# Kernel optimization log

Measured on AMD Instinct MI355X. Metric: run time of the kernel, lower is better.

The kernel has to match this reference:

```python
import jax, jax.numpy as jnp
import numpy as np

N_NODES = 50000


def graph_conv(x, W, b, src, dst, n_nodes):
    # DGL GraphConv with norm='both': h = D_in^{-1/2} A D_out^{-1/2} x W + b
    ones = jnp.ones(src.shape[0], dtype=x.dtype)
    deg_out = jax.ops.segment_sum(ones, src, num_segments=n_nodes)
    deg_in = jax.ops.segment_sum(ones, dst, num_segments=n_nodes)
    norm_out = jnp.power(jnp.clip(deg_out, 1.0, None), -0.5)
    norm_in = jnp.power(jnp.clip(deg_in, 1.0, None), -0.5)
    x = x * norm_out[:, None]
    msgs = x[src]                                   # [E, d] gather
    agg = jax.ops.segment_sum(msgs, dst, num_segments=n_nodes)  # [N, d] scatter-add
    agg = agg * norm_in[:, None]
    return agg @ W + b


def setup_inputs() -> dict:
    key = jax.random.key(0)
    ks = jax.random.split(key, 16)
    d = 128
    h = 2 * d
    od = 64
    E = 800000
    T = 4096

    def lin(k, fan_in, fan_out):
        bound = 1.0 / np.sqrt(fan_in)
        k1, k2 = jax.random.split(k)
        W = jax.random.uniform(k1, (fan_in, fan_out), jnp.float32, -bound, bound)
        b = jax.random.uniform(k2, (fan_out,), jnp.float32, -bound, bound)
        return W, b

    features = jax.random.normal(ks[0], (N_NODES, d), jnp.float32)
    src = jax.random.randint(ks[1], (E,), 0, N_NODES)
    dst = jax.random.randint(ks[2], (E,), 0, N_NODES)
    trigger_nodes = jax.random.randint(ks[3], (T,), 0, N_NODES)

    W1, b1 = lin(ks[4], d, h)
    W2, b2 = lin(ks[5], h, d)
    Wf, bf = lin(ks[6], d, d)
    Wf1, bf1 = lin(ks[7], d, d)
    We, be = lin(ks[8], d, od)
    We1, be1 = lin(ks[9], od, od)

    return {
        "features": features, "src": src, "dst": dst,
        "trigger_nodes": trigger_nodes,
        "W1": W1, "b1": b1, "W2": W2, "b2": b2,
        "Wf": Wf, "bf": bf, "Wf1": Wf1, "bf1": bf1,
        "We": We, "be": be, "We1": We1, "be1": be1,
    }


def reference(features, src, dst, trigger_nodes,
              W1, b1, W2, b2, Wf, bf, Wf1, bf1, We, be, We1, be1):
    n = features.shape[0]
    h = jax.nn.relu(graph_conv(features, W1, b1, src, dst, n))   # [N, 2d]
    h = jax.nn.relu(graph_conv(h, W2, b2, src, dst, n))          # [N, d]
    ht = h[trigger_nodes]                                        # [T, d] gather
    feat = jax.nn.relu(ht @ Wf + bf) @ Wf1 + bf1                 # [T, d]
    edge_weight = jax.nn.relu(ht @ We + be) @ We1 + be1          # [T, od]
    return (feat, edge_weight)
```

## Files before the change

### kernel.cpp

```cpp
#include <hip/hip_runtime.h>
#include <hip/hip_bf16.h>


typedef __attribute__((ext_vector_type(8))) short short8;
typedef __attribute__((ext_vector_type(4))) float f32x4;

#define NQ_CAP 12544

union U16B { uint4 u; short8 s; };

__device__ __forceinline__ unsigned pack_hl(float v)
{
    unsigned u = __builtin_bit_cast(unsigned, v);
    unsigned rb = u + 0x7fffu + ((u >> 16) & 1u);
    float hf = __builtin_bit_cast(float, rb & 0xffff0000u);
    float r = v - hf;
    unsigned l = __builtin_bit_cast(unsigned, r) & 0xffff0000u;
    return (rb >> 16) | l;
}

__device__ __forceinline__ float decode_hl(unsigned u)
{
    float hf = __builtin_bit_cast(float, u << 16);
    float lf = __builtin_bit_cast(float, u & 0xffff0000u);
    return hf + lf;
}

__device__ __forceinline__ void unpack_hl(uint4 a, uint4 b, short8& h, short8& l)
{
    U16B H, L;
    H.u.x = (a.x & 0xffffu) | (a.y << 16);
    H.u.y = (a.z & 0xffffu) | (a.w << 16);
    H.u.z = (b.x & 0xffffu) | (b.y << 16);
    H.u.w = (b.z & 0xffffu) | (b.w << 16);
    L.u.x = (a.x >> 16) | (a.y & 0xffff0000u);
    L.u.y = (a.z >> 16) | (a.w & 0xffff0000u);
    L.u.z = (b.x >> 16) | (b.y & 0xffff0000u);
    L.u.w = (b.z >> 16) | (b.w & 0xffff0000u);
    h = H.s; l = L.s;
}

__global__ __launch_bounds__(256) void hist_kernel(
    const int* __restrict__ src, const int* __restrict__ dst,
    unsigned* __restrict__ part_in, unsigned* __restrict__ part_out,
    int E, int chunk, int nq)
{
    __shared__ unsigned c32[NQ_CAP];
    const int b = blockIdx.x;
    const int* __restrict__ idx = blockIdx.y ? src : dst;
    unsigned* __restrict__ part = blockIdx.y ? part_out : part_in;

    for (int i = threadIdx.x; i < nq; i += 256) c32[i] = 0u;
    __syncthreads();

    const int base = b * chunk;
    const int lim = min(base + chunk, E);
    for (int e = base + threadIdx.x; e < lim; e += 256) {
        int n = idx[e];
        atomicAdd(&c32[n >> 2], 1u << ((n & 3) * 8));
    }
    __syncthreads();

    unsigned* __restrict__ o = part + (long)b * nq;
    for (int i = threadIdx.x; i < nq; i += 256) o[i] = c32[i];
}

__global__ __launch_bounds__(256) void merge_kernel(
    unsigned* __restrict__ part_in, const unsigned* __restrict__ part_out,
    int* __restrict__ deg_in, float* __restrict__ norm_in,
    float* __restrict__ norm_out, int nq, int N)
{
    __shared__ unsigned gsum[4][64];
    const int il = threadIdx.x & 63;
    const int bg = threadIdx.x >> 6;
    const int i = blockIdx.x * 64 + il;
    const bool valid = (i < nq);

    unsigned p[32];
    unsigned run = 0u;
    if (valid) {
        #pragma unroll
        for (int j = 0; j < 32; ++j)
            p[j] = part_in[(long)(bg * 32 + j) * nq + i];
        #pragma unroll
        for (int j = 0; j < 32; ++j) run += p[j];
    }
    gsum[bg][il] = run;
    __syncthreads();

    unsigned base = 0u;
    #pragma unroll
    for (int g = 0; g < 4; ++g) {
        unsigned v = gsum[g][il];
        if (g < bg) base += v;
    }

    unsigned ro = 0u;
    if (valid) {
        #pragma unroll
        for (int j = 0; j < 32; ++j)
            ro += part_out[(long)(bg * 32 + j) * nq + i];
    }

    if (valid) {
        unsigned acc = base;
        #pragma unroll
        for (int j = 0; j < 32; ++j) {
            part_in[(long)(bg * 32 + j) * nq + i] = acc;
            acc += p[j];
        }
        if (bg == 3) {
            #pragma unroll
            for (int k = 0; k < 4; ++k) {
                int n = 4 * i + k;
                if (n < N) {
                    int dk = (int)((acc >> (8 * k)) & 0xffu);
                    deg_in[n] = dk;
                    norm_in[n] = rsqrtf(fmaxf((float)dk, 1.0f));
                }
            }
        }
    }

    __syncthreads();
    gsum[bg][il] = ro;
    __syncthreads();
    if (valid && bg == 0) {
        unsigned rt = gsum[0][il] + gsum[1][il] + gsum[2][il] + gsum[3][il];
        #pragma unroll
        for (int k = 0; k < 4; ++k) {
            int n = 4 * i + k;
            if (n < N)
                norm_out[n] = rsqrtf(fmaxf((float)((rt >> (8 * k)) & 0xffu), 1.0f));
        }
    }
}

__global__ __launch_bounds__(256) void scan1_kernel(
    const int* __restrict__ deg, int* __restrict__ rowptr,
    int* __restrict__ bsum, int N)
{
    __shared__ int s[256];
    int t = threadIdx.x;
    int i = blockIdx.x * 256 + t;
    s[t] = (i < N) ? deg[i] : 0;
    __syncthreads();
    #pragma unroll
    for (int off = 1; off < 256; off <<= 1) {
        int v = (t >= off) ? s[t - off] : 0;
        __syncthreads();
        s[t] += v;
        __syncthreads();
    }
    if (i < N) rowptr[i + 1] = s[t];
    if (t == 255) bsum[blockIdx.x] = s[255];
}

__global__ __launch_bounds__(256) void scan2_kernel(int* __restrict__ bsum, int nb)
{
    __shared__ int s[256];
    int t = threadIdx.x;
    s[t] = (t < nb) ? bsum[t] : 0;
    __syncthreads();
    #pragma unroll
    for (int off = 1; off < 256; off <<= 1) {
        int v = (t >= off) ? s[t - off] : 0;
        __syncthreads();
        s[t] += v;
        __syncthreads();
    }
    if (t < nb) bsum[t] = s[t];
}

__global__ __launch_bounds__(256) void scan3_kernel(
    int* __restrict__ rowptr, const int* __restrict__ bsum, int N)
{
    int b = blockIdx.x;
    int i = b * 256 + threadIdx.x;
    if (i < N) {
        int add = (b > 0) ? bsum[b - 1] : 0;
        rowptr[i + 1] += add;
    }
    if (i == 0) rowptr[0] = 0;
}

__global__ __launch_bounds__(256) void fill2_kernel(
    const int* __restrict__ src, const int* __restrict__ dst,
    const int* __restrict__ rowptr, const unsigned* __restrict__ part_in,
    int* __restrict__ ecol, int E, int chunk, int nq)
{
    __shared__ unsigned c32[NQ_CAP];
    const int b = blockIdx.x;
    const unsigned* __restrict__ pref = part_in + (long)b * nq;
    for (int i = threadIdx.x; i < nq; i += 256) c32[i] = pref[i];
    __syncthreads();

    const int base = b * chunk;
    const int lim = min(base + chunk, E);
    for (int e = base + threadIdx.x; e < lim; e += 256) {
        int r = dst[e];
        unsigned old = atomicAdd(&c32[r >> 2], 1u << ((r & 3) * 8));
        unsigned slot = (old >> ((r & 3) * 8)) & 0xffu;
        ecol[rowptr[r] + (int)slot] = src[e];
    }
}

struct WPrep {
    const float* w[6];
    unsigned* o[6];
    int K[6], N[6], dstK[6], base[7];
};

__global__ __launch_bounds__(256) void wprep_kernel(WPrep p)
{
    int t = blockIdx.x * 256 + threadIdx.x;
    if (t >= p.base[6]) return;
    int s = 0;
    while (t >= p.base[s + 1]) ++s;
    int loc = t - p.base[s];
    int K = p.K[s], N = p.N[s];
    int n = loc / K, k = loc - n * K;
    p.o[s][(long)n * p.dstK[s] + k] = pack_hl(p.w[s][(long)k * N + n]);
}

__global__ __launch_bounds__(256) void gather4_kernel(
    const float* __restrict__ x, const float* __restrict__ nsrc,
    const int* __restrict__ rowptr, const int* __restrict__ ecol,
    unsigned* __restrict__ out, int N)
{
    const int wave = threadIdx.x >> 6;
    const int lane = threadIdx.x & 63;
    const int r = blockIdx.x * 4 + wave;
    if (r >= N) return;
    const int q = lane & 31;
    const int h = lane >> 5;
    const int beg = rowptr[r], end = rowptr[r + 1];
    const float4* __restrict__ x4 = (const float4*)x;

    float4 acc = make_float4(0.f, 0.f, 0.f, 0.f);
    int k = beg + h;
    int sA = (k < end) ? ecol[k] : -1;
    int sB = (k + 2 < end) ? ecol[k + 2] : -1;
    float4 vA = make_float4(0.f, 0.f, 0.f, 0.f), vB = vA;
    float nA = 0.f, nB = 0.f;
    if (sA >= 0) { vA = x4[(long)sA * 32 + q]; nA = nsrc[sA]; }
    if (sB >= 0) { vB = x4[(long)sB * 32 + q]; nB = nsrc[sB]; }
    while (sA >= 0) {
        int sC = (k + 4 < end) ? ecol[k + 4] : -1;
        float4 vC = make_float4(0.f, 0.f, 0.f, 0.f);
        float nC = 0.f;
        if (sC >= 0) { vC = x4[(long)sC * 32 + q]; nC = nsrc[sC]; }
        acc.x = fmaf(vA.x, nA, acc.x);
        acc.y = fmaf(vA.y, nA, acc.y);
        acc.z = fmaf(vA.z, nA, acc.z);
        acc.w = fmaf(vA.w, nA, acc.w);
        sA = sB; vA = vB; nA = nB;
        sB = sC; vB = vC; nB = nC;
        k += 2;
    }
    acc.x += __shfl(acc.x, lane ^ 32);
    acc.y += __shfl(acc.y, lane ^ 32);
    acc.z += __shfl(acc.z, lane ^ 32);
    acc.w += __shfl(acc.w, lane ^ 32);
    if (h == 0) {
        uint4 o;
        o.x = pack_hl(acc.x); o.y = pack_hl(acc.y);
        o.z = pack_hl(acc.z); o.w = pack_hl(acc.w);
        *reinterpret_cast<uint4*>(&out[(long)r * 128 + q * 4]) = o;
    }
}

__global__ __launch_bounds__(256) void gather_trig256_kernel(
    const unsigned* __restrict__ h1s, const int* __restrict__ trig,
    const float* __restrict__ norm_in,
    const int* __restrict__ rowptr, const int* __restrict__ ecol,
    unsigned* __restrict__ agg2ts, int T)
{
    const int wave = threadIdx.x >> 6;
    const int lane = threadIdx.x & 63;
    const int b = blockIdx.x * 4 + wave;
    if (b >= T) return;
    const int r = trig[b];
    const int beg = rowptr[r], end = rowptr[r + 1];
    const uint4* __restrict__ h4 = (const uint4*)h1s;

    float4 acc = make_float4(0.f, 0.f, 0.f, 0.f);
    int k = beg;
    int sA = (k < end) ? ecol[k] : -1;
    int sB = (k + 1 < end) ? ecol[k + 1] : -1;
    uint4 vA = make_uint4(0u, 0u, 0u, 0u), vB = vA;
    if (sA >= 0) vA = h4[(long)sA * 64 + lane];
    if (sB >= 0) vB = h4[(long)sB * 64 + lane];
    while (sA >= 0) {
        int sC = (k + 2 < end) ? ecol[k + 2] : -1;
        uint4 vC = make_uint4(0u, 0u, 0u, 0u);
        if (sC >= 0) vC = h4[(long)sC * 64 + lane];
        acc.x += decode_hl(vA.x);
        acc.y += decode_hl(vA.y);
        acc.z += decode_hl(vA.z);
        acc.w += decode_hl(vA.w);
        sA = sB; vA = vB;
        sB = sC; vB = vC;
        ++k;
    }
    const float ni = norm_in[r];
    uint4 o;
    o.x = pack_hl(acc.x * ni); o.y = pack_hl(acc.y * ni);
    o.z = pack_hl(acc.z * ni); o.w = pack_hl(acc.w * ni);
    *reinterpret_cast<uint4*>(&agg2ts[(long)b * 256 + lane * 4]) = o;
}

__global__ __launch_bounds__(256) void mgemm256_kernel(
    const unsigned* __restrict__ A, const unsigned* __restrict__ Bp,
    const float* __restrict__ bias, const float* __restrict__ ni,
    const float* __restrict__ no, unsigned* __restrict__ Cp, int M)
{
    constexpr int K = 128;
    const int tid = threadIdx.x;
    const int lane = tid & 63, wave = tid >> 6;
    const int l15 = lane & 15, l4 = lane >> 4;
    const int row0 = blockIdx.x * 128;

    long aof[2];
    #pragma unroll
    for (int i = 0; i < 2; ++i) {
        int r = row0 + wave * 32 + i * 16 + l15;
        if (r > M - 1) r = M - 1;
        aof[i] = (long)r * K + l4 * 8;
    }
    const long bbase = (long)l15 * K + l4 * 8;

    uint4 abuf[2][2][2];
    #pragma unroll
    for (int i = 0; i < 2; ++i) {
        abuf[0][i][0] = *reinterpret_cast<const uint4*>(&A[aof[i] + 0]);
        abuf[0][i][1] = *reinterpret_cast<const uint4*>(&A[aof[i] + 4]);
        abuf[1][i][0] = *reinterpret_cast<const uint4*>(&A[aof[i] + 32]);
        abuf[1][i][1] = *reinterpret_cast<const uint4*>(&A[aof[i] + 36]);
    }

    f32x4 acc[2][16];
    #pragma unroll
    for (int i = 0; i < 2; ++i)
        #pragma unroll
        for (int j = 0; j < 16; ++j)
            acc[i][j] = (f32x4){0.f, 0.f, 0.f, 0.f};

    uint4 bq[4][2];
    #pragma unroll
    for (int t0 = 0; t0 < 4; ++t0) {
        const long na = bbase + (long)(t0 & 15) * 16 * K + (t0 >> 4) * 32;
        bq[t0][0] = *reinterpret_cast<const uint4*>(&Bp[na]);
        bq[t0][1] = *reinterpret_cast<const uint4*>(&Bp[na + 4]);
    }

    short8 ah[2], al[2];

    #pragma unroll
    for (int t = 0; t < 64; ++t) {
        const int c = t >> 4, j = t & 15;
        if (j == 0) {
            const int cp = c & 1;
            unpack_hl(abuf[cp][0][0], abuf[cp][0][1], ah[0], al[0]);
            unpack_hl(abuf[cp][1][0], abuf[cp][1][1], ah[1], al[1]);
            if (c + 2 < 4) {
                #pragma unroll
                for (int i = 0; i < 2; ++i) {
                    abuf[cp][i][0] = *reinterpret_cast<const uint4*>(&A[aof[i] + (c + 2) * 32]);
                    abuf[cp][i][1] = *reinterpret_cast<const uint4*>(&A[aof[i] + (c + 2) * 32 + 4]);
                }
            }
        }
        short8 bh, bl;
        unpack_hl(bq[t & 3][0], bq[t & 3][1], bh, bl);
        if (t + 4 < 64) {
            const int c1 = (t + 4) >> 4, j1 = (t + 4) & 15;
            const long na = bbase + (long)j1 * 16 * K + c1 * 32;
            bq[t & 3][0] = *reinterpret_cast<const uint4*>(&Bp[na]);
            bq[t & 3][1] = *reinterpret_cast<const uint4*>(&Bp[na + 4]);
        }
        #pragma unroll
        for (int i = 0; i < 2; ++i) {
            acc[i][j] = __builtin_amdgcn_mfma_f32_16x16x32_bf16(ah[i], bh, acc[i][j], 0, 0, 0);
            acc[i][j] = __builtin_amdgcn_mfma_f32_16x16x32_bf16(ah[i], bl, acc[i][j], 0, 0, 0);
            acc[i][j] = __builtin_amdgcn_mfma_f32_16x16x32_bf16(al[i], bh, acc[i][j], 0, 0, 0);
        }
    }

    #pragma unroll
    for (int i = 0; i < 2; ++i) {
        const int rbase = row0 + wave * 32 + i * 16 + l4 * 4;
        #pragma unroll
        for (int g = 0; g < 4; ++g) {
            const int row = rbase + g;
            if (row >= M) continue;
            const float niv = ni[row], nov = no[row];
            #pragma unroll
            for (int j = 0; j < 16; ++j) {
                const int col = j * 16 + l15;
                float v = fmaxf(fmaf(niv, acc[i][j][g], bias[col]), 0.f) * nov;
                Cp[(long)row * 256 + col] = pack_hl(v);
            }
        }
    }
}

template<int TN, bool RELU, bool PACK_OUT>
__global__ __launch_bounds__(256) void mgemm_kernel(
    const unsigned* __restrict__ A, const unsigned* __restrict__ Bp,
    const float* __restrict__ bias, const float* __restrict__ bias2,
    const float* __restrict__ rowscale, const float* __restrict__ outscale,
    float* __restrict__ C, unsigned* __restrict__ Cp, int M, int N, int K)
{
    constexpr int IM = 2, KC = 32, TM = 128;
    constexpr int JF = TN / 16;
    constexpr int BLD = (TN * KC) / (4 * 256);

    __shared__ unsigned sB[KC * TN];

    const int tid = threadIdx.x;
    const int lane = tid & 63;
    const int wave = tid >> 6;
    const int l15 = lane & 15, l4 = lane >> 4;
    const int row0 = blockIdx.y * TM;
    const int col0 = blockIdx.x * TN;

    int bro[BLD], bgr[BLD];
    long bof[BLD];
    #pragma unroll
    for (int l = 0; l < BLD; ++l) {
        int idx = tid + 256 * l;
        bro[l] = idx % TN;
        bgr[l] = idx / TN;
        bof[l] = (long)(col0 + bro[l]) * K + bgr[l] * 4;
    }
    long aof[IM];
    #pragma unroll
    for (int i = 0; i < IM; ++i) {
        int r = row0 + wave * 32 + i * 16 + l15;
        if (r > M - 1) r = M - 1;
        aof[i] = (long)r * K + l4 * 8;
    }

    uint4 cB[BLD], nB[BLD], cA[IM][2], nA[IM][2];
    #pragma unroll
    for (int l = 0; l < BLD; ++l)
        cB[l] = *reinterpret_cast<const uint4*>(&Bp[bof[l]]);
    #pragma unroll
    for (int i = 0; i < IM; ++i) {
        cA[i][0] = *reinterpret_cast<const uint4*>(&A[aof[i]]);
        cA[i][1] = *reinterpret_cast<const uint4*>(&A[aof[i] + 4]);
    }

    f32x4 acc[IM][JF];
    #pragma unroll
    for (int i = 0; i < IM; ++i)
        #pragma unroll
        for (int j = 0; j < JF; ++j)
            acc[i][j] = (f32x4){0.f, 0.f, 0.f, 0.f};

    const int nc = K / KC;
    for (int c = 0; c < nc; ++c) {
        #pragma unroll
        for (int l = 0; l < BLD; ++l)
            *reinterpret_cast<uint4*>(&sB[(bgr[l] * TN + bro[l]) * 4]) = cB[l];
        __syncthreads();

        if (c + 1 < nc) {
            const int kc = (c + 1) * KC;
            #pragma unroll
            for (int l = 0; l < BLD; ++l)
                nB[l] = *reinterpret_cast<const uint4*>(&Bp[bof[l] + kc]);
            #pragma unroll
            for (int i = 0; i < IM; ++i) {
                nA[i][0] = *reinterpret_cast<const uint4*>(&A[aof[i] + kc]);
                nA[i][1] = *reinterpret_cast<const uint4*>(&A[aof[i] + kc + 4]);
            }
        }

        short8 ah[IM], al[IM];
        #pragma unroll
        for (int i = 0; i < IM; ++i)
            unpack_hl(cA[i][0], cA[i][1], ah[i], al[i]);

        #pragma unroll
        for (int j = 0; j < JF; ++j) {
            const int rowb = j * 16 + l15;
            uint4 b0 = *reinterpret_cast<const uint4*>(&sB[((2 * l4 + 0) * TN + rowb) * 4]);
            uint4 b1 = *reinterpret_cast<const uint4*>(&sB[((2 * l4 + 1) * TN + rowb) * 4]);
            short8 bh, bl;
            unpack_hl(b0, b1, bh, bl);
            #pragma unroll
            for (int i = 0; i < IM; ++i) {
                acc[i][j] = __builtin_amdgcn_mfma_f32_16x16x32_bf16(ah[i], bh, acc[i][j], 0, 0, 0);
                acc[i][j] = __builtin_amdgcn_mfma_f32_16x16x32_bf16(ah[i], bl, acc[i][j], 0, 0, 0);
                acc[i][j] = __builtin_amdgcn_mfma_f32_16x16x32_bf16(al[i], bh, acc[i][j], 0, 0, 0);
            }
        }
        __syncthreads();

        if (c + 1 < nc) {
            #pragma unroll
            for (int l = 0; l < BLD; ++l) cB[l] = nB[l];
            #pragma unroll
            for (int i = 0; i < IM; ++i) { cA[i][0] = nA[i][0]; cA[i][1] = nA[i][1]; }
        }
    }

    #pragma unroll
    for (int i = 0; i < IM; ++i) {
        const int rb = row0 + wave * 32 + i * 16 + l4 * 4;
        #pragma unroll
        for (int j = 0; j < JF; ++j) {
            const int col = col0 + j * 16 + l15;
            float bs = 0.0f;
            if (bias) bs = (bias2 && col >= 128) ? bias2[col - 128] : bias[col];
            #pragma unroll
            for (int g = 0; g < 4; ++g) {
                const int row = rb + g;
                if (row >= M) continue;
                float v = acc[i][j][g];
                if (rowscale) v *= rowscale[row];
                v += bs;
                if (RELU) v = fmaxf(v, 0.0f);
                if (outscale) v *= outscale[row];
                if (PACK_OUT) Cp[(long)row * N + col] = pack_hl(v);
                else          C[(long)row * N + col] = v;
            }
        }
    }
}

__global__ __launch_bounds__(256) void mgemm_heads_kernel(
    const unsigned* __restrict__ A, const unsigned* __restrict__ Bp,
    const float* __restrict__ bf1, const float* __restrict__ be1,
    float* __restrict__ Cf, float* __restrict__ Ce, int M)
{
    constexpr int IM = 2, KC = 32, TM = 128, TN = 64, K = 192;
    constexpr int JF = TN / 16;
    constexpr int BLD = (TN * KC) / (4 * 256);

    __shared__ unsigned sB[KC * TN];

    const int tid = threadIdx.x;
    const int lane = tid & 63;
    const int wave = tid >> 6;
    const int l15 = lane & 15, l4 = lane >> 4;
    const int row0 = blockIdx.y * TM;
    const int col0 = blockIdx.x * TN;

    int bro[BLD], bgr[BLD];
    long bof[BLD];
    #pragma unroll
    for (int l = 0; l < BLD; ++l) {
        int idx = tid + 256 * l;
        bro[l] = idx % TN;
        bgr[l] = idx / TN;
        bof[l] = (long)(col0 + bro[l]) * K + bgr[l] * 4;
    }
    long aof[IM];
    #pragma unroll
    for (int i = 0; i < IM; ++i) {
        int r = row0 + wave * 32 + i * 16 + l15;
        if (r > M - 1) r = M - 1;
        aof[i] = (long)r * K + l4 * 8;
    }

    uint4 cB[BLD], nB[BLD], cA[IM][2], nA[IM][2];
    #pragma unroll
    for (int l = 0; l < BLD; ++l)
        cB[l] = *reinterpret_cast<const uint4*>(&Bp[bof[l]]);
    #pragma unroll
    for (int i = 0; i < IM; ++i) {
        cA[i][0] = *reinterpret_cast<const uint4*>(&A[aof[i]]);
        cA[i][1] = *reinterpret_cast<const uint4*>(&A[aof[i] + 4]);
    }

    f32x4 acc[IM][JF];
    #pragma unroll
    for (int i = 0; i < IM; ++i)
        #pragma unroll
        for (int j = 0; j < JF; ++j)
            acc[i][j] = (f32x4){0.f, 0.f, 0.f, 0.f};

    const int nc = K / KC;
    for (int c = 0; c < nc; ++c) {
        #pragma unroll
        for (int l = 0; l < BLD; ++l)
            *reinterpret_cast<uint4*>(&sB[(bgr[l] * TN + bro[l]) * 4]) = cB[l];
        __syncthreads();

        if (c + 1 < nc) {
            const int kc = (c + 1) * KC;
            #pragma unroll
            for (int l = 0; l < BLD; ++l)
                nB[l] = *reinterpret_cast<const uint4*>(&Bp[bof[l] + kc]);
            #pragma unroll
            for (int i = 0; i < IM; ++i) {
                nA[i][0] = *reinterpret_cast<const uint4*>(&A[aof[i] + kc]);
                nA[i][1] = *reinterpret_cast<const uint4*>(&A[aof[i] + kc + 4]);
            }
        }

        short8 ah[IM], al[IM];
        #pragma unroll
        for (int i = 0; i < IM; ++i)
            unpack_hl(cA[i][0], cA[i][1], ah[i], al[i]);

        #pragma unroll
        for (int j = 0; j < JF; ++j) {
            const int rowb = j * 16 + l15;
            uint4 b0 = *reinterpret_cast<const uint4*>(&sB[((2 * l4 + 0) * TN + rowb) * 4]);
            uint4 b1 = *reinterpret_cast<const uint4*>(&sB[((2 * l4 + 1) * TN + rowb) * 4]);
            short8 bh, bl;
            unpack_hl(b0, b1, bh, bl);
            #pragma unroll
            for (int i = 0; i < IM; ++i) {
                acc[i][j] = __builtin_amdgcn_mfma_f32_16x16x32_bf16(ah[i], bh, acc[i][j], 0, 0, 0);
                acc[i][j] = __builtin_amdgcn_mfma_f32_16x16x32_bf16(ah[i], bl, acc[i][j], 0, 0, 0);
                acc[i][j] = __builtin_amdgcn_mfma_f32_16x16x32_bf16(al[i], bh, acc[i][j], 0, 0, 0);
            }
        }
        __syncthreads();

        if (c + 1 < nc) {
            #pragma unroll
            for (int l = 0; l < BLD; ++l) cB[l] = nB[l];
            #pragma unroll
            for (int i = 0; i < IM; ++i) { cA[i][0] = nA[i][0]; cA[i][1] = nA[i][1]; }
        }
    }

    #pragma unroll
    for (int i = 0; i < IM; ++i) {
        const int rb = row0 + wave * 32 + i * 16 + l4 * 4;
        #pragma unroll
        for (int j = 0; j < JF; ++j) {
            const int col = col0 + j * 16 + l15;
            const bool isf = (col < 128);
            const float bs = isf ? bf1[col] : be1[col - 128];
            #pragma unroll
            for (int g = 0; g < 4; ++g) {
                const int row = rb + g;
                if (row >= M) continue;
                float v = acc[i][j][g] + bs;
                if (isf) Cf[(long)row * 128 + col] = v;
                else     Ce[(long)row * 64 + (col - 128)] = v;
            }
        }
    }
}

static inline long align8(long x) { return (x + 7) & ~7L; }

extern "C" void kernel_launch(void* const* d_in, const int* in_sizes, int n_in,
                              void* d_out, int out_size, void* d_ws, size_t ws_size,
                              hipStream_t stream)
{
    const float* features = (const float*)d_in[0];
    const int*   src      = (const int*)d_in[1];
    const int*   dst      = (const int*)d_in[2];
    const int*   trig     = (const int*)d_in[3];
    const float* W1  = (const float*)d_in[4];
    const float* b1  = (const float*)d_in[5];
    const float* W2  = (const float*)d_in[6];
    const float* b2  = (const float*)d_in[7];
    const float* Wf  = (const float*)d_in[8];
    const float* bf  = (const float*)d_in[9];
    const float* Wf1 = (const float*)d_in[10];
    const float* bf1 = (const float*)d_in[11];
    const float* We  = (const float*)d_in[12];
    const float* be  = (const float*)d_in[13];
    const float* We1 = (const float*)d_in[14];
    const float* be1 = (const float*)d_in[15];

    const int  d   = 128, h2d = 256, od = 64;
    const int  N   = in_sizes[0] / d;
    const int  E   = in_sizes[1];
    const int  T   = in_sizes[3];
    const int  NB  = (N + 255) / 256;

    const int  HB    = 128;
    const int  chunk = (E + HB - 1) / HB;
    const int  nq    = (N + 3) / 4;

    char* wsb = (char*)d_ws;
    long off = 0;
    auto takeF = [&](long n) { float* p = (float*)(wsb + off); off += align8(n) * 4; return p; };
    auto takeI = [&](long n) { int*   p = (int*)  (wsb + off); off += align8(n) * 4; return p; };
    auto takeU = [&](long n) { unsigned* p = (unsigned*)(wsb + off); off += align8(n) * 4; return p; };

    float*    norm_out = takeF(N);
    float*    norm_in  = takeF(N);
    int*      deg_in   = takeI(N);
    int*      rowptr   = takeI(N + 1);
    int*      bsum     = takeI(256);
    int*      ecol     = takeI(E);
    unsigned* part_in  = takeU((long)HB * nq);
    unsigned* part_out = takeU((long)HB * nq);
    unsigned* agg1     = takeU((long)N * d);
    unsigned* h1s      = takeU((long)N * h2d);
    unsigned* agg2ts   = takeU((long)T * h2d);
    unsigned* h2t      = takeU((long)T * d);
    unsigned* tmpc     = takeU((long)T * 192);
    unsigned* w1p      = takeU((long)h2d * d);
    unsigned* w2p      = takeU((long)d * h2d);
    unsigned* wc       = takeU(192L * d);
    unsigned* wd1      = takeU(192L * 192);

    float* out_feat = (float*)d_out;
    float* out_edge = out_feat + (long)T * d;

    hipMemsetAsync(wd1, 0, 192L * 192 * sizeof(unsigned), stream);
    WPrep wp;
    wp.w[0] = W1;  wp.o[0] = w1p;              wp.K[0] = d;   wp.N[0] = h2d; wp.dstK[0] = d;
    wp.w[1] = W2;  wp.o[1] = w2p;              wp.K[1] = h2d; wp.N[1] = d;   wp.dstK[1] = h2d;
    wp.w[2] = Wf;  wp.o[2] = wc;               wp.K[2] = d;   wp.N[2] = d;   wp.dstK[2] = d;
    wp.w[3] = We;  wp.o[3] = wc + 128 * d;     wp.K[3] = d;   wp.N[3] = od;  wp.dstK[3] = d;
    wp.w[4] = Wf1; wp.o[4] = wd1;              wp.K[4] = d;   wp.N[4] = d;   wp.dstK[4] = 192;
    wp.w[5] = We1; wp.o[5] = wd1 + 128L * 192 + 128;
                                               wp.K[5] = od;  wp.N[5] = od;  wp.dstK[5] = 192;
    wp.base[0] = 0;
    for (int i = 0; i < 6; ++i) wp.base[i + 1] = wp.base[i] + wp.K[i] * wp.N[i];
    wprep_kernel<<<dim3((wp.base[6] + 255) / 256), dim3(256), 0, stream>>>(wp);

    hist_kernel<<<dim3(HB, 2), dim3(256), 0, stream>>>(
        src, dst, part_in, part_out, E, chunk, nq);
    merge_kernel<<<dim3((nq + 63) / 64), dim3(256), 0, stream>>>(
        part_in, part_out, deg_in, norm_in, norm_out, nq, N);
    scan1_kernel<<<dim3(NB), dim3(256), 0, stream>>>(deg_in, rowptr, bsum, N);
    scan2_kernel<<<dim3(1), dim3(256), 0, stream>>>(bsum, NB);
    scan3_kernel<<<dim3(NB), dim3(256), 0, stream>>>(rowptr, bsum, N);
    fill2_kernel<<<dim3(HB), dim3(256), 0, stream>>>(
        src, dst, rowptr, part_in, ecol, E, chunk, nq);

    const int GY = (N + 127) / 128;
    const int GT = T / 128;

    gather4_kernel<<<dim3((N + 3) / 4), dim3(256), 0, stream>>>(
        features, norm_out, rowptr, ecol, agg1, N);
    mgemm256_kernel<<<dim3(GY), dim3(256), 0, stream>>>(
        agg1, w1p, b1, norm_in, norm_out, h1s, N);

    gather_trig256_kernel<<<dim3((T + 3) / 4), dim3(256), 0, stream>>>(
        h1s, trig, norm_in, rowptr, ecol, agg2ts, T);
    mgemm_kernel<64, true, true><<<dim3(d / 64, GT), dim3(256), 0, stream>>>(
        agg2ts, w2p, b2, nullptr, nullptr, nullptr, nullptr, h2t, T, d, h2d);

    mgemm_kernel<64, true, true><<<dim3(192 / 64, GT), dim3(256), 0, stream>>>(
        h2t, wc, bf, be, nullptr, nullptr, nullptr, tmpc, T, 192, d);
    mgemm_heads_kernel<<<dim3(3, GT), dim3(256), 0, stream>>>(
        tmpc, wd1, bf1, be1, out_feat, out_edge, T);
}
```

Before: 270.9 us.

## Fuse first-layer neighbor gather into the W1 GEMM via shared memory

Replaces the separate gather kernel and the MFMA GEMM with one kernel. Each 128-row block first aggregates its rows' neighbor features into a swizzled LDS tile, then runs the split-bf16 MFMA GEMM from LDS. This removes the global agg1 intermediate write and read and one launch. In exchange, each wave gathers 32 rows serially and the grid shrinks to about N/128 blocks with 64KB LDS each, which cuts parallelism for the latency-bound gather.

```diff
diff --git a/kernel.cpp b/kernel.cpp
--- a/kernel.cpp
+++ b/kernel.cpp
@@ -223,50 +223,129 @@
     p.o[s][(long)n * p.dstK[s] + k] = pack_hl(p.w[s][(long)k * N + n]);
 }
 
-__global__ __launch_bounds__(256) void gather4_kernel(
+__global__ __launch_bounds__(256) void fused1_kernel(
     const float* __restrict__ x, const float* __restrict__ nsrc,
     const int* __restrict__ rowptr, const int* __restrict__ ecol,
-    unsigned* __restrict__ out, int N)
-{
-    const int wave = threadIdx.x >> 6;
-    const int lane = threadIdx.x & 63;
-    const int r = blockIdx.x * 4 + wave;
-    if (r >= N) return;
-    const int q = lane & 31;
-    const int h = lane >> 5;
-    const int beg = rowptr[r], end = rowptr[r + 1];
-    const float4* __restrict__ x4 = (const float4*)x;
-
-    float4 acc = make_float4(0.f, 0.f, 0.f, 0.f);
-    int k = beg + h;
-    int sA = (k < end) ? ecol[k] : -1;
-    int sB = (k + 2 < end) ? ecol[k + 2] : -1;
-    float4 vA = make_float4(0.f, 0.f, 0.f, 0.f), vB = vA;
-    float nA = 0.f, nB = 0.f;
-    if (sA >= 0) { vA = x4[(long)sA * 32 + q]; nA = nsrc[sA]; }
-    if (sB >= 0) { vB = x4[(long)sB * 32 + q]; nB = nsrc[sB]; }
-    while (sA >= 0) {
-        int sC = (k + 4 < end) ? ecol[k + 4] : -1;
-        float4 vC = make_float4(0.f, 0.f, 0.f, 0.f);
-        float nC = 0.f;
-        if (sC >= 0) { vC = x4[(long)sC * 32 + q]; nC = nsrc[sC]; }
-        acc.x = fmaf(vA.x, nA, acc.x);
-        acc.y = fmaf(vA.y, nA, acc.y);
-        acc.z = fmaf(vA.z, nA, acc.z);
-        acc.w = fmaf(vA.w, nA, acc.w);
-        sA = sB; vA = vB; nA = nB;
-        sB = sC; vB = vC; nB = nC;
-        k += 2;
-    }
-    acc.x += __shfl(acc.x, lane ^ 32);
-    acc.y += __shfl(acc.y, lane ^ 32);
-    acc.z += __shfl(acc.z, lane ^ 32);
-    acc.w += __shfl(acc.w, lane ^ 32);
-    if (h == 0) {
-        uint4 o;
-        o.x = pack_hl(acc.x); o.y = pack_hl(acc.y);
-        o.z = pack_hl(acc.z); o.w = pack_hl(acc.w);
-        *reinterpret_cast<uint4*>(&out[(long)r * 128 + q * 4]) = o;
+    const unsigned* __restrict__ Bp, const float* __restrict__ bias,
+    const float* __restrict__ ni, const float* __restrict__ no,
+    unsigned* __restrict__ Cp, int N)
+{
+    constexpr int K = 128;
+    __shared__ unsigned sA[128 * 128];
+
+    const int tid = threadIdx.x;
+    const int lane = tid & 63, wave = tid >> 6;
+    const int row0 = blockIdx.x * 128;
+
+    {
+        const int q = lane & 31;
+        const int h = lane >> 5;
+        const float4* __restrict__ x4 = (const float4*)x;
+        for (int rr = 0; rr < 32; ++rr) {
+            const int slot = wave * 32 + rr;
+            const int r = row0 + slot;
+            float4 acc = make_float4(0.f, 0.f, 0.f, 0.f);
+            if (r < N) {
+                const int beg = rowptr[r], end = rowptr[r + 1];
+                int k = beg + h;
+                int sAi = (k < end) ? ecol[k] : -1;
+                int sBi = (k + 2 < end) ? ecol[k + 2] : -1;
+                float4 vA = make_float4(0.f, 0.f, 0.f, 0.f), vB = vA;
+                float nA = 0.f, nB = 0.f;
+                if (sAi >= 0) { vA = x4[(long)sAi * 32 + q]; nA = nsrc[sAi]; }
+                if (sBi >= 0) { vB = x4[(long)sBi * 32 + q]; nB = nsrc[sBi]; }
+                while (sAi >= 0) {
+                    int sCi = (k + 4 < end) ? ecol[k + 4] : -1;
+                    float4 vC = make_float4(0.f, 0.f, 0.f, 0.f);
+                    float nC = 0.f;
+                    if (sCi >= 0) { vC = x4[(long)sCi * 32 + q]; nC = nsrc[sCi]; }
+                    acc.x = fmaf(vA.x, nA, acc.x);
+                    acc.y = fmaf(vA.y, nA, acc.y);
+                    acc.z = fmaf(vA.z, nA, acc.z);
+                    acc.w = fmaf(vA.w, nA, acc.w);
+                    sAi = sBi; vA = vB; nA = nB;
+                    sBi = sCi; vB = vC; nB = nC;
+                    k += 2;
+                }
+            }
+            acc.x += __shfl(acc.x, lane ^ 32);
+            acc.y += __shfl(acc.y, lane ^ 32);
+            acc.z += __shfl(acc.z, lane ^ 32);
+            acc.w += __shfl(acc.w, lane ^ 32);
+            if (h == 0) {
+                uint4 o;
+                o.x = pack_hl(acc.x); o.y = pack_hl(acc.y);
+                o.z = pack_hl(acc.z); o.w = pack_hl(acc.w);
+                const int g = q >> 1, sub = q & 1;
+                const int swzg = g ^ (slot & 3);
+                *reinterpret_cast<uint4*>(&sA[slot * 128 + swzg * 8 + sub * 4]) = o;
+            }
+        }
+    }
+    __syncthreads();
+
+    const int l15 = lane & 15, l4 = lane >> 4;
+    const long bbase = (long)l15 * K + l4 * 8;
+
+    f32x4 acc[2][16];
+    #pragma unroll
+    for (int i = 0; i < 2; ++i)
+        #pragma unroll
+        for (int j = 0; j < 16; ++j)
+            acc[i][j] = (f32x4){0.f, 0.f, 0.f, 0.f};
+
+    short8 ah[2], al[2];
+    uint4 b0 = *reinterpret_cast<const uint4*>(&Bp[bbase]);
+    uint4 b1 = *reinterpret_cast<const uint4*>(&Bp[bbase + 4]);
+
+    #pragma unroll
+    for (int t = 0; t < 64; ++t) {
+        const int c = t >> 4, j = t & 15;
+        if (j == 0) {
+            #pragma unroll
+            for (int i = 0; i < 2; ++i) {
+                const int slot = wave * 32 + i * 16 + l15;
+                const int g = c * 4 + l4;
+                const int swzg = g ^ (slot & 3);
+                const int off = slot * 128 + swzg * 8;
+                uint4 a0 = *reinterpret_cast<const uint4*>(&sA[off]);
+                uint4 a1 = *reinterpret_cast<const uint4*>(&sA[off + 4]);
+                unpack_hl(a0, a1, ah[i], al[i]);
+            }
+        }
+        uint4 nb0, nb1;
+        if (t + 1 < 64) {
+            const int c1 = (t + 1) >> 4, j1 = (t + 1) & 15;
+            const long na = bbase + (long)j1 * 16 * K + c1 * 32;
+            nb0 = *reinterpret_cast<const uint4*>(&Bp[na]);
+            nb1 = *reinterpret_cast<const uint4*>(&Bp[na + 4]);
+        }
+        short8 bh, bl;
+        unpack_hl(b0, b1, bh, bl);
+        #pragma unroll
+        for (int i = 0; i < 2; ++i) {
+            acc[i][j] = __builtin_amdgcn_mfma_f32_16x16x32_bf16(ah[i], bh, acc[i][j], 0, 0, 0);
+            acc[i][j] = __builtin_amdgcn_mfma_f32_16x16x32_bf16(ah[i], bl, acc[i][j], 0, 0, 0);
+            acc[i][j] = __builtin_amdgcn_mfma_f32_16x16x32_bf16(al[i], bh, acc[i][j], 0, 0, 0);
+        }
+        b0 = nb0; b1 = nb1;
+    }
+
+    #pragma unroll
+    for (int i = 0; i < 2; ++i) {
+        const int rbase = row0 + wave * 32 + i * 16 + l4 * 4;
+        #pragma unroll
+        for (int g = 0; g < 4; ++g) {
+            const int row = rbase + g;
+            if (row >= N) continue;
+            const float niv = ni[row], nov = no[row];
+            #pragma unroll
+            for (int j = 0; j < 16; ++j) {
+                const int col = j * 16 + l15;
+                float v = fmaxf(fmaf(niv, acc[i][j][g], bias[col]), 0.f) * nov;
+                Cp[(long)row * 256 + col] = pack_hl(v);
+            }
+        }
     }
 }
 
@@ -310,101 +389,6 @@
     *reinterpret_cast<uint4*>(&agg2ts[(long)b * 256 + lane * 4]) = o;
 }
 
-__global__ __launch_bounds__(256) void mgemm256_kernel(
-    const unsigned* __restrict__ A, const unsigned* __restrict__ Bp,
-    const float* __restrict__ bias, const float* __restrict__ ni,
-    const float* __restrict__ no, unsigned* __restrict__ Cp, int M)
-{
-    constexpr int K = 128;
-    const int tid = threadIdx.x;
-    const int lane = tid & 63, wave = tid >> 6;
-    const int l15 = lane & 15, l4 = lane >> 4;
-    const int row0 = blockIdx.x * 128;
-
-    long aof[2];
-    #pragma unroll
-    for (int i = 0; i < 2; ++i) {
-        int r = row0 + wave * 32 + i * 16 + l15;
-        if (r > M - 1) r = M - 1;
-        aof[i] = (long)r * K + l4 * 8;
-    }
-    const long bbase = (long)l15 * K + l4 * 8;
-
-    uint4 abuf[2][2][2];
-    #pragma unroll
-    for (int i = 0; i < 2; ++i) {
-        abuf[0][i][0] = *reinterpret_cast<const uint4*>(&A[aof[i] + 0]);
-        abuf[0][i][1] = *reinterpret_cast<const uint4*>(&A[aof[i] + 4]);
-        abuf[1][i][0] = *reinterpret_cast<const uint4*>(&A[aof[i] + 32]);
-        abuf[1][i][1] = *reinterpret_cast<const uint4*>(&A[aof[i] + 36]);
-    }
-
-    f32x4 acc[2][16];
-    #pragma unroll
-    for (int i = 0; i < 2; ++i)
-        #pragma unroll
-        for (int j = 0; j < 16; ++j)
-            acc[i][j] = (f32x4){0.f, 0.f, 0.f, 0.f};
-
-    uint4 bq[4][2];
-    #pragma unroll
-    for (int t0 = 0; t0 < 4; ++t0) {
-        const long na = bbase + (long)(t0 & 15) * 16 * K + (t0 >> 4) * 32;
-        bq[t0][0] = *reinterpret_cast<const uint4*>(&Bp[na]);
-        bq[t0][1] = *reinterpret_cast<const uint4*>(&Bp[na + 4]);
-    }
-
-    short8 ah[2], al[2];
-
-    #pragma unroll
-    for (int t = 0; t < 64; ++t) {
-        const int c = t >> 4, j = t & 15;
-        if (j == 0) {
-            const int cp = c & 1;
-            unpack_hl(abuf[cp][0][0], abuf[cp][0][1], ah[0], al[0]);
-            unpack_hl(abuf[cp][1][0], abuf[cp][1][1], ah[1], al[1]);
-            if (c + 2 < 4) {
-                #pragma unroll
-                for (int i = 0; i < 2; ++i) {
-                    abuf[cp][i][0] = *reinterpret_cast<const uint4*>(&A[aof[i] + (c + 2) * 32]);
-                    abuf[cp][i][1] = *reinterpret_cast<const uint4*>(&A[aof[i] + (c + 2) * 32 + 4]);
-                }
-            }
-        }
-        short8 bh, bl;
-        unpack_hl(bq[t & 3][0], bq[t & 3][1], bh, bl);
-        if (t + 4 < 64) {
-            const int c1 = (t + 4) >> 4, j1 = (t + 4) & 15;
-            const long na = bbase + (long)j1 * 16 * K + c1 * 32;
-            bq[t & 3][0] = *reinterpret_cast<const uint4*>(&Bp[na]);
-            bq[t & 3][1] = *reinterpret_cast<const uint4*>(&Bp[na + 4]);
-        }
-        #pragma unroll
-        for (int i = 0; i < 2; ++i) {
-            acc[i][j] = __builtin_amdgcn_mfma_f32_16x16x32_bf16(ah[i], bh, acc[i][j], 0, 0, 0);
-            acc[i][j] = __builtin_amdgcn_mfma_f32_16x16x32_bf16(ah[i], bl, acc[i][j], 0, 0, 0);
-            acc[i][j] = __builtin_amdgcn_mfma_f32_16x16x32_bf16(al[i], bh, acc[i][j], 0, 0, 0);
-        }
-    }
-
-    #pragma unroll
-    for (int i = 0; i < 2; ++i) {
-        const int rbase = row0 + wave * 32 + i * 16 + l4 * 4;
-        #pragma unroll
-        for (int g = 0; g < 4; ++g) {
-            const int row = rbase + g;
-            if (row >= M) continue;
-            const float niv = ni[row], nov = no[row];
-            #pragma unroll
-            for (int j = 0; j < 16; ++j) {
-                const int col = j * 16 + l15;
-                float v = fmaxf(fmaf(niv, acc[i][j][g], bias[col]), 0.f) * nov;
-                Cp[(long)row * 256 + col] = pack_hl(v);
-            }
-        }
-    }
-}
-
 template<int TN, bool RELU, bool PACK_OUT>
 __global__ __launch_bounds__(256) void mgemm_kernel(
     const unsigned* __restrict__ A, const unsigned* __restrict__ Bp,
@@ -698,7 +682,6 @@
     int*      ecol     = takeI(E);
     unsigned* part_in  = takeU((long)HB * nq);
     unsigned* part_out = takeU((long)HB * nq);
-    unsigned* agg1     = takeU((long)N * d);
     unsigned* h1s      = takeU((long)N * h2d);
     unsigned* agg2ts   = takeU((long)T * h2d);
     unsigned* h2t      = takeU((long)T * d);
@@ -737,10 +720,8 @@
     const int GY = (N + 127) / 128;
     const int GT = T / 128;
 
-    gather4_kernel<<<dim3((N + 3) / 4), dim3(256), 0, stream>>>(
-        features, norm_out, rowptr, ecol, agg1, N);
-    mgemm256_kernel<<<dim3(GY), dim3(256), 0, stream>>>(
-        agg1, w1p, b1, norm_in, norm_out, h1s, N);
+    fused1_kernel<<<dim3(GY), dim3(256), 0, stream>>>(
+        features, norm_out, rowptr, ecol, w1p, b1, norm_in, norm_out, h1s, N);
 
     gather_trig256_kernel<<<dim3((T + 3) / 4), dim3(256), 0, stream>>>(
         h1s, trig, norm_in, rowptr, ecol, agg2ts, T);
```

After: 480.6 us. +77.4%, slower.
